# Optimization experiments

Hardware: AMD Instinct MI355X
Metric: run time of the kernel (lower is better)

The kernel has to match this reference:

```python
import jax, jax.numpy as jnp
import numpy as np

N_NODES = 50000
N_EDGES = 600000
D_NODE_IN = 32
D_EDGE_IN = 16
H = 128
D_OUT = 2
N_PASSES = 5
LN_EPS = 1e-6  # flax LayerNorm default


def _dense(key, fan_in, fan_out, scale=0.05):
    return (jax.random.normal(key, (fan_in, fan_out), dtype=jnp.float32) * scale)


def setup_inputs() -> dict:
    key = jax.random.key(0)
    ks = jax.random.split(key, 16)
    inp = {
        "nodes": jax.random.normal(ks[0], (N_NODES, D_NODE_IN), dtype=jnp.float32),
        "edges": jax.random.normal(ks[1], (N_EDGES, D_EDGE_IN), dtype=jnp.float32),
        "senders": jax.random.randint(ks[2], (N_EDGES,), 0, N_NODES, dtype=jnp.int32),
        "receivers": jax.random.randint(ks[3], (N_EDGES,), 0, N_NODES, dtype=jnp.int32),
        # node encoder ReluMLP [128,128]
        "enc_n_W0": _dense(ks[4], D_NODE_IN, H), "enc_n_b0": jnp.zeros((H,), jnp.float32),
        "enc_n_W1": _dense(ks[5], H, H), "enc_n_b1": jnp.zeros((H,), jnp.float32),
        # edge encoder ReluMLP [128,128]
        "enc_e_W0": _dense(ks[6], D_EDGE_IN, H), "enc_e_b0": jnp.zeros((H,), jnp.float32),
        "enc_e_W1": _dense(ks[7], H, H), "enc_e_b1": jnp.zeros((H,), jnp.float32),
        # weight-tied LinearMessagePassingLayer params
        "W_msg": _dense(ks[8], H + H, H),                 # Dense(no bias) on concat(sender_feat, edge)
        "node_W0": _dense(ks[9], H + H, H), "node_b0": jnp.zeros((H,), jnp.float32),
        "node_W1": _dense(ks[10], H, H), "node_b1": jnp.zeros((H,), jnp.float32),
        "W_node": _dense(ks[11], H, H),                   # residual projection, no bias
        "ln_g": jnp.ones((H,), jnp.float32), "ln_b": jnp.zeros((H,), jnp.float32),
        # node decoder ReluMLP [128,2]
        "dec_W0": _dense(ks[12], H, H), "dec_b0": jnp.zeros((H,), jnp.float32),
        "dec_W1": _dense(ks[13], H, D_OUT), "dec_b1": jnp.zeros((D_OUT,), jnp.float32),
    }
    return inp


def _relu_mlp(x, layers):
    # Dense+ReLU for all but last layer; last layer linear.
    n = len(layers)
    for i, (W, b) in enumerate(layers):
        x = x @ W + b
        if i < n - 1:
            x = jax.nn.relu(x)
    return x


def _layer_norm(x, g, b):
    mu = jnp.mean(x, axis=-1, keepdims=True)
    var = jnp.var(x, axis=-1, keepdims=True)
    return (x - mu) * jax.lax.rsqrt(var + LN_EPS) * g + b


def reference(nodes, edges, senders, receivers,
              enc_n_W0, enc_n_b0, enc_n_W1, enc_n_b1,
              enc_e_W0, enc_e_b0, enc_e_W1, enc_e_b1,
              W_msg, node_W0, node_b0, node_W1, node_b1,
              W_node, ln_g, ln_b,
              dec_W0, dec_b0, dec_W1, dec_b1):
    n = _relu_mlp(nodes, [(enc_n_W0, enc_n_b0), (enc_n_W1, enc_n_b1)])  # [N,H]
    e = _relu_mlp(edges, [(enc_e_W0, enc_e_b0), (enc_e_W1, enc_e_b1)])  # [E,H]
    total_nodes = n.shape[0]

    for _ in range(N_PASSES):  # weight-tied process block
        sender_features = n[senders]                                    # gather [E,H]
        msg_in = jnp.concatenate([sender_features, e], axis=-1)         # [E,2H]
        messages = msg_in @ W_msg                                       # [E,H]
        agg = jax.ops.segment_sum(messages, receivers, num_segments=total_nodes)
        node_in = jnp.concatenate([n, agg], axis=-1)                    # [N,2H]
        nodes_out = _relu_mlp(node_in, [(node_W0, node_b0), (node_W1, node_b1)])
        n = _layer_norm(n @ W_node + nodes_out, ln_g, ln_b)

    return _relu_mlp(n, [(dec_W0, dec_b0), (dec_W1, dec_b1)])           # [N,2]
```

## Files before the change

### kernel.cpp

```cpp
#include <hip/hip_runtime.h>

#define DEVFN __device__ __forceinline__

namespace {

constexpr int NN = 50000;
constexpr int NE = 600000;
constexpr int H  = 128;
constexpr float LN_EPS = 1e-6f;

typedef _Float16 f16x8 __attribute__((ext_vector_type(8)));
typedef _Float16 f16x4 __attribute__((ext_vector_type(4)));
typedef float f32x4 __attribute__((ext_vector_type(4)));

DEVFN void mm_block(const float* xsrow, int pitch, int K,
                    const float* __restrict__ W, int c0, float (&acc)[8][4]) {
  for (int k = 0; k < K; k += 4) {
    float4 w0 = *(const float4*)(W + (size_t)(k + 0) * H + c0);
    float4 w1 = *(const float4*)(W + (size_t)(k + 1) * H + c0);
    float4 w2 = *(const float4*)(W + (size_t)(k + 2) * H + c0);
    float4 w3 = *(const float4*)(W + (size_t)(k + 3) * H + c0);
#pragma unroll
    for (int r = 0; r < 8; ++r) {
      float4 a = *(const float4*)(xsrow + r * pitch + k);
      acc[r][0] += a.x * w0.x; acc[r][0] += a.y * w1.x; acc[r][0] += a.z * w2.x; acc[r][0] += a.w * w3.x;
      acc[r][1] += a.x * w0.y; acc[r][1] += a.y * w1.y; acc[r][1] += a.z * w2.y; acc[r][1] += a.w * w3.y;
      acc[r][2] += a.x * w0.z; acc[r][2] += a.y * w1.z; acc[r][2] += a.z * w2.z; acc[r][2] += a.w * w3.z;
      acc[r][3] += a.x * w0.w; acc[r][3] += a.y * w1.w; acc[r][3] += a.z * w2.w; acc[r][3] += a.w * w3.w;
    }
  }
}

DEVFN void linear_body(const float* __restrict__ x, const float* __restrict__ W,
                       float* __restrict__ y, int r0, int R, int t, float* xs) {
  {
    const int r = t & 31, q = t >> 5;
    int row = r0 + r;
    if (row >= R) row = R - 1;
    const float* src = &x[(size_t)row * H + q * 32];
#pragma unroll
    for (int j = 0; j < 8; ++j)
      *(float4*)&xs[r * 132 + q * 32 + j * 4] = *(const float4*)&src[j * 4];
  }
  __syncthreads();
  const int c0 = (t & 31) * 4;
  const int rbase = (t >> 5) * 8;
  float acc[8][4];
#pragma unroll
  for (int r = 0; r < 8; ++r) { acc[r][0] = 0.f; acc[r][1] = 0.f; acc[r][2] = 0.f; acc[r][3] = 0.f; }
  mm_block(&xs[rbase * 132], 132, H, W, c0, acc);
#pragma unroll
  for (int r = 0; r < 8; ++r) {
    int row = r0 + rbase + r;
    if (row < R)
      *(float4*)&y[(size_t)row * H + c0] =
          make_float4(acc[r][0], acc[r][1], acc[r][2], acc[r][3]);
  }
}

__global__ __launch_bounds__(128) void fold1_kernel(
    const float* __restrict__ Wb, const float* __restrict__ Wt,
    const float* __restrict__ W0b, float* __restrict__ T,
    float* __restrict__ Wf) {
  __shared__ float xs[32 * 132];
  const float* x = (blockIdx.x < 4) ? Wb : Wt;
  float* y = (blockIdx.x < 4) ? T : Wf;
  linear_body(x, W0b, y, (blockIdx.x & 3) * 32, 128, threadIdx.x, xs);
}

__global__ __launch_bounds__(128) void fold2_kernel(
    const float* __restrict__ W1e, const float* __restrict__ b1e,
    const float* __restrict__ T, float* __restrict__ Wc2,
    float* __restrict__ bc2) {
  __shared__ float xs[32 * 132];
  if (blockIdx.x < 4) {
    linear_body(W1e, T, Wc2, blockIdx.x * 32, 128, threadIdx.x, xs);
  } else {
    int j = threadIdx.x;
    float s = 0.f;
    for (int k = 0; k < H; ++k) s += b1e[k] * T[(size_t)k * H + j];
    bc2[j] = s;
  }
}

__global__ __launch_bounds__(64) void prepack7_kernel(
    const float* __restrict__ s0, const float* __restrict__ s1,
    const float* __restrict__ s2, const float* __restrict__ s3,
    const float* __restrict__ s4, const float* __restrict__ s5,
    const float* __restrict__ s6, _Float16* __restrict__ pkBase) {
  const int z = blockIdx.z;
  const float* W = (z == 0) ? s0 : (z == 1) ? s1 : (z == 2) ? s2 :
                   (z == 3) ? s3 : (z == 4) ? s4 : (z == 5) ? s5 : s6;
  _Float16* pk = pkBase + (size_t)z * 128 * H;
  const int ks = blockIdx.x, ct = blockIdx.y, l = threadIdx.x;
  const int kbase = ks * 32 + (l >> 4) * 8;
  const int col = ct * 16 + (l & 15);
  _Float16 tmp[8];
#pragma unroll
  for (int j = 0; j < 8; ++j)
    tmp[j] = (_Float16)W[(size_t)(kbase + j) * H + col];
  *(f16x8*)&pk[((size_t)((ks * 8 + ct) * 64) + l) * 8] = *(f16x8*)tmp;
}

__global__ __launch_bounds__(64) void prepack_w0e_kernel(
    const float* __restrict__ W0e, _Float16* __restrict__ pk) {
  const int ct = blockIdx.x, l = threadIdx.x;
  const int quad = l >> 4;
  const int col = ct * 16 + (l & 15);
  _Float16 tmp[8];
#pragma unroll
  for (int j = 0; j < 8; ++j) {
    int k = quad * 8 + j;
    tmp[j] = (quad < 2) ? (_Float16)W0e[(size_t)k * H + col] : (_Float16)0.f;
  }
  *(f16x8*)&pk[((size_t)(ct * 64) + l) * 8] = *(f16x8*)tmp;
}

__global__ __launch_bounds__(64) void prepack_k32_kernel(
    const float* __restrict__ W, _Float16* __restrict__ pk) {
  const int ct = blockIdx.x, l = threadIdx.x;
  const int quad = l >> 4;
  const int col = ct * 16 + (l & 15);
  _Float16 tmp[8];
#pragma unroll
  for (int j = 0; j < 8; ++j)
    tmp[j] = (_Float16)W[(size_t)(quad * 8 + j) * H + col];
  *(f16x8*)&pk[((size_t)(ct * 64) + l) * 8] = *(f16x8*)tmp;
}

__global__ __launch_bounds__(256) void hist_kernel(const int* __restrict__ recv,
                                                   int* __restrict__ cnt) {
  int i = blockIdx.x * 256 + threadIdx.x;
  if (i < NE) atomicAdd(&cnt[recv[i]], 1);
}

__global__ __launch_bounds__(256) void scan1_kernel(const int* __restrict__ cnt,
                                                    int* __restrict__ excl,
                                                    int* __restrict__ part) {
  __shared__ int s[256];
  int t = threadIdx.x;
  int i = blockIdx.x * 256 + t;
  int v = (i < NN) ? cnt[i] : 0;
  s[t] = v;
  __syncthreads();
  for (int off = 1; off < 256; off <<= 1) {
    int x = (t >= off) ? s[t - off] : 0;
    __syncthreads();
    s[t] += x;
    __syncthreads();
  }
  if (i < NN) excl[i] = s[t] - v;
  if (t == 255) part[blockIdx.x] = s[255];
}

__global__ __launch_bounds__(256) void scan2_kernel(int* __restrict__ part, int nb) {
  __shared__ int s[256];
  int t = threadIdx.x;
  int v = (t < nb) ? part[t] : 0;
  s[t] = v;
  __syncthreads();
  for (int off = 1; off < 256; off <<= 1) {
    int x = (t >= off) ? s[t - off] : 0;
    __syncthreads();
    s[t] += x;
    __syncthreads();
  }
  if (t < nb) part[t] = s[t] - v;
}

__global__ __launch_bounds__(256) void scan3_kernel(int* __restrict__ excl,
                                                    const int* __restrict__ part,
                                                    int* __restrict__ cursor) {
  int i = blockIdx.x * 256 + threadIdx.x;
  if (i < NN) {
    int e = excl[i] + part[i >> 8];
    excl[i] = e;
    cursor[i] = e;
  }
}

__global__ __launch_bounds__(256) void scatter_permute_kernel(
    const int* __restrict__ senders, const int* __restrict__ recv,
    int* __restrict__ cursor, const float* __restrict__ edges,
    int* __restrict__ sendp, _Float16* __restrict__ edgesP16) {
  const int t = threadIdx.x;
  const int i = blockIdx.x * 64 + (t >> 2);
  if (i >= NE) return;
  const int sub = t & 3;
  int pos = 0;
  if (sub == 0) pos = atomicAdd(&cursor[recv[i]], 1);
  pos = __shfl(pos, (t & 63) & ~3);
  if (sub == 0) sendp[pos] = senders[i];
  float4 v = *(const float4*)&edges[(size_t)i * 16 + sub * 4];
  f16x4 h = {(_Float16)v.x, (_Float16)v.y, (_Float16)v.z, (_Float16)v.w};
  *(f16x4*)&edgesP16[(size_t)pos * 16 + sub * 4] = h;
}

__global__ __launch_bounds__(256) void encoder_mfma_kernel(
    const float* __restrict__ x, const float* __restrict__ b0,
    const float* __restrict__ b1, const _Float16* __restrict__ pkEW0,
    const _Float16* __restrict__ pkEW1, _Float16* __restrict__ outp) {
  __shared__ _Float16 lds[4][16 * 136];
  const int t = threadIdx.x;
  const int wave = t >> 6, lane = t & 63;
  const int row0 = blockIdx.x * 64 + wave * 16;
  const int quad = lane >> 4, m16 = lane & 15;
  _Float16* hlds = &lds[wave][0];

  int arow = row0 + m16;
  if (arow >= NN) arow = NN - 1;
  f16x8 a0;
  {
    const float* src = &x[(size_t)arow * 32 + quad * 8];
    float4 v0 = *(const float4*)(src);
    float4 v1 = *(const float4*)(src + 4);
    a0[0] = (_Float16)v0.x; a0[1] = (_Float16)v0.y;
    a0[2] = (_Float16)v0.z; a0[3] = (_Float16)v0.w;
    a0[4] = (_Float16)v1.x; a0[5] = (_Float16)v1.y;
    a0[6] = (_Float16)v1.z; a0[7] = (_Float16)v1.w;
  }
#pragma unroll
  for (int ct = 0; ct < 8; ++ct) {
    float bb = b0[ct * 16 + m16];
    f32x4 acc = (f32x4){bb, bb, bb, bb};
    acc = __builtin_amdgcn_mfma_f32_16x16x32_f16(
        a0, *(const f16x8*)&pkEW0[((size_t)(ct * 64) + lane) * 8], acc, 0, 0, 0);
#pragma unroll
    for (int q = 0; q < 4; ++q)
      hlds[(quad * 4 + q) * 136 + ct * 16 + m16] = (_Float16)fmaxf(acc[q], 0.f);
  }
  __syncthreads();
  const _Float16* hrow = &hlds[m16 * 136 + quad * 8];
  f16x8 ah[4];
#pragma unroll
  for (int ks = 0; ks < 4; ++ks) ah[ks] = *(const f16x8*)(hrow + ks * 32);
  f32x4 acc2[8];
#pragma unroll
  for (int ct = 0; ct < 8; ++ct) {
    float bb = b1[ct * 16 + m16];
    acc2[ct] = (f32x4){bb, bb, bb, bb};
  }
#pragma unroll
  for (int ks = 0; ks < 4; ++ks) {
    const _Float16* bp = pkEW1 + ((size_t)ks * 8 * 64 + lane) * 8;
#pragma unroll
    for (int ct = 0; ct < 8; ++ct)
      acc2[ct] = __builtin_amdgcn_mfma_f32_16x16x32_f16(
          ah[ks], *(const f16x8*)(bp + ct * 512), acc2[ct], 0, 0, 0);
  }
  __syncthreads();
#pragma unroll
  for (int ct = 0; ct < 8; ++ct)
#pragma unroll
    for (int q = 0; q < 4; ++q)
      hlds[(quad * 4 + q) * 136 + ct * 16 + m16] = (_Float16)acc2[ct][q];
  __syncthreads();
  {
    int lr = lane >> 2, cc = (lane & 3) * 32;
    int orow = row0 + lr;
    if (orow < NN) {
      const _Float16* src = &hlds[lr * 136 + cc];
      _Float16* dst = &outp[(size_t)orow * H + cc];
      *(f16x8*)(dst + 0)  = *(const f16x8*)(src + 0);
      *(f16x8*)(dst + 8)  = *(const f16x8*)(src + 8);
      *(f16x8*)(dst + 16) = *(const f16x8*)(src + 16);
      *(f16x8*)(dst + 24) = *(const f16x8*)(src + 24);
    }
  }
}

__global__ __launch_bounds__(256) void hs_mfma_kernel(
    const _Float16* __restrict__ edgesP16, const int* __restrict__ start,
    const int* __restrict__ endc, const _Float16* __restrict__ pkW0e,
    const float* __restrict__ b0e, float* __restrict__ Hs) {
  const int t = threadIdx.x;
  const int wave = t >> 6, lane = t & 63;
  const int v = blockIdx.x * 4 + wave;
  const int quad = lane >> 4, m16 = lane & 15;
  const int j0 = start[v];
  const int deg = endc[v] - j0;

  float binit[8];
#pragma unroll
  for (int ct = 0; ct < 8; ++ct) binit[ct] = b0e[ct * 16 + m16];
  f16x8 bfrag[8];
#pragma unroll
  for (int ct = 0; ct < 8; ++ct)
    bfrag[ct] = *(const f16x8*)&pkW0e[((size_t)(ct * 64) + lane) * 8];

  float rsum[8][4];
#pragma unroll
  for (int ct = 0; ct < 8; ++ct)
#pragma unroll
    for (int q = 0; q < 4; ++q) rsum[ct][q] = 0.f;

  for (int base = 0; base < deg; base += 16) {
    f16x8 a = {};
    if (quad < 2 && base + m16 < deg)
      a = *(const f16x8*)&edgesP16[(size_t)(j0 + base + m16) * 16 + quad * 8];
#pragma unroll
    for (int ct = 0; ct < 8; ++ct) {
      f32x4 acc = (f32x4){binit[ct], binit[ct], binit[ct], binit[ct]};
      acc = __builtin_amdgcn_mfma_f32_16x16x32_f16(a, bfrag[ct], acc, 0, 0, 0);
#pragma unroll
      for (int q = 0; q < 4; ++q) {
        int row = quad * 4 + q;
        float hv = fmaxf(acc[q], 0.f);
        rsum[ct][q] += (base + row < deg) ? hv : 0.f;
      }
    }
  }
#pragma unroll
  for (int ct = 0; ct < 8; ++ct) {
    float s = (rsum[ct][0] + rsum[ct][1]) + (rsum[ct][2] + rsum[ct][3]);
    s += __shfl_xor(s, 16);
    s += __shfl_xor(s, 32);
    if (lane < 16) Hs[(size_t)v * H + ct * 16 + lane] = s;
  }
}

__global__ __launch_bounds__(256) void blinpack_mfma_kernel(
    const float* __restrict__ Hs, const _Float16* __restrict__ pkWc2,
    const float* __restrict__ bc2, const int* __restrict__ start,
    const int* __restrict__ endc, _Float16* __restrict__ B2pk) {
  const int t = threadIdx.x;
  const int wave = t >> 6, lane = t & 63;
  const int tile = blockIdx.x * 4 + wave;
  const int row0 = tile * 16;
  const int quad = lane >> 4, m16 = lane & 15;
  int arow = row0 + m16;
  if (arow >= NN) arow = NN - 1;
  f16x8 ah[4];
#pragma unroll
  for (int ks = 0; ks < 4; ++ks) {
    const float* src = &Hs[(size_t)arow * H + ks * 32 + quad * 8];
    float4 v0 = *(const float4*)src;
    float4 v1 = *(const float4*)(src + 4);
    f16x8 a;
    a[0] = (_Float16)v0.x; a[1] = (_Float16)v0.y;
    a[2] = (_Float16)v0.z; a[3] = (_Float16)v0.w;
    a[4] = (_Float16)v1.x; a[5] = (_Float16)v1.y;
    a[6] = (_Float16)v1.z; a[7] = (_Float16)v1.w;
    ah[ks] = a;
  }
  float degq[4];
#pragma unroll
  for (int q = 0; q < 4; ++q) {
    int r = row0 + quad * 4 + q;
    degq[q] = (r < NN) ? (float)(endc[r] - start[r]) : 0.f;
  }
  f32x4 acc[8];
#pragma unroll
  for (int ct = 0; ct < 8; ++ct) {
    float bcv = bc2[ct * 16 + m16];
    acc[ct] = (f32x4){degq[0] * bcv, degq[1] * bcv, degq[2] * bcv, degq[3] * bcv};
  }
#pragma unroll
  for (int ks = 0; ks < 4; ++ks) {
    const _Float16* bp = pkWc2 + ((size_t)ks * 8 * 64 + lane) * 8;
#pragma unroll
    for (int ct = 0; ct < 8; ++ct)
      acc[ct] = __builtin_amdgcn_mfma_f32_16x16x32_f16(
          ah[ks], *(const f16x8*)(bp + ct * 512), acc[ct], 0, 0, 0);
  }
  _Float16 tmp[32];
#pragma unroll
  for (int ct = 0; ct < 8; ++ct)
#pragma unroll
    for (int q = 0; q < 4; ++q) tmp[ct * 4 + q] = (_Float16)acc[ct][q];
  _Float16* dst = &B2pk[((size_t)tile * 64 + lane) * 32];
#pragma unroll
  for (int i = 0; i < 4; ++i)
    *(f16x8*)(dst + i * 8) = *(f16x8*)(tmp + i * 8);
}

__global__ __launch_bounds__(256) void gather_kernel(
    const _Float16* __restrict__ n16, const int* __restrict__ start,
    const int* __restrict__ endc, const int* __restrict__ sendp,
    _Float16* __restrict__ S) {
  const int t = threadIdx.x;
  const int v = blockIdx.x * 4 + (t >> 6);
  const int lane = t & 63;
  const int grp = lane >> 4;
  const int c = (lane & 15) * 8;
  float a[8] = {0.f, 0.f, 0.f, 0.f, 0.f, 0.f, 0.f, 0.f};
  const int e = endc[v];
  int j = start[v];
  for (; j + 7 < e; j += 8) {
    int s0 = sendp[j + grp];
    int s1 = sendp[j + 4 + grp];
    f16x8 p0 = *(const f16x8*)&n16[(size_t)s0 * H + c];
    f16x8 p1 = *(const f16x8*)&n16[(size_t)s1 * H + c];
#pragma unroll
    for (int i = 0; i < 8; ++i) a[i] += (float)p0[i] + (float)p1[i];
  }
  for (; j < e; j += 4) {
    int jj = j + grp;
    if (jj < e) {
      int s0 = sendp[jj];
      f16x8 p0 = *(const f16x8*)&n16[(size_t)s0 * H + c];
#pragma unroll
      for (int i = 0; i < 8; ++i) a[i] += (float)p0[i];
    }
  }
#pragma unroll
  for (int i = 0; i < 8; ++i) {
    a[i] += __shfl_xor(a[i], 16);
    a[i] += __shfl_xor(a[i], 32);
  }
  if (lane < 16) {
    f16x8 o;
#pragma unroll
    for (int i = 0; i < 8; ++i) o[i] = (_Float16)a[i];
    *(f16x8*)&S[(size_t)v * H + c] = o;
  }
}

__global__ __launch_bounds__(256) void node_mfma_kernel(
    const _Float16* __restrict__ n16, const _Float16* __restrict__ S16,
    const _Float16* __restrict__ B2pk,
    const _Float16* __restrict__ pkW0t, const _Float16* __restrict__ pkWf,
    const float* __restrict__ b0,
    const _Float16* __restrict__ pkW1, const _Float16* __restrict__ pkWn,
    const float* __restrict__ b1,
    const float* __restrict__ ln_g, const float* __restrict__ ln_b,
    _Float16* __restrict__ nout) {
  __shared__ _Float16 lds[4][16 * 136];
  const int t = threadIdx.x;
  const int wave = t >> 6, lane = t & 63;
  const int row0 = blockIdx.x * 64 + wave * 16;
  const int quad = lane >> 4, m16 = lane & 15;
  _Float16* hlds = &lds[wave][0];

  int arow = row0 + m16;
  if (arow >= NN) arow = NN - 1;
  const _Float16* nrow = &n16[(size_t)arow * H + quad * 8];
  const _Float16* srow = &S16[(size_t)arow * H + quad * 8];
  f16x8 an[4], as[4];
#pragma unroll
  for (int ks = 0; ks < 4; ++ks) {
    an[ks] = *(const f16x8*)(nrow + ks * 32);
    as[ks] = *(const f16x8*)(srow + ks * 32);
  }

  const int tile = blockIdx.x * 4 + wave;
  const _Float16* b2l = &B2pk[((size_t)tile * 64 + lane) * 32];
  f32x4 acc[8];
#pragma unroll
  for (int ct = 0; ct < 8; ++ct) {
    float bb = b0[ct * 16 + m16];
    f16x4 bv = *(const f16x4*)(b2l + ct * 4);
    acc[ct] = (f32x4){bb + (float)bv[0], bb + (float)bv[1],
                      bb + (float)bv[2], bb + (float)bv[3]};
  }
#pragma unroll
  for (int ks = 0; ks < 4; ++ks) {
    const _Float16* bp0 = pkW0t + ((size_t)ks * 8 * 64 + lane) * 8;
    const _Float16* bpf = pkWf + ((size_t)ks * 8 * 64 + lane) * 8;
#pragma unroll
    for (int ct = 0; ct < 8; ++ct) {
      f16x8 bw0 = *(const f16x8*)(bp0 + ct * 512);
      acc[ct] = __builtin_amdgcn_mfma_f32_16x16x32_f16(an[ks], bw0, acc[ct], 0, 0, 0);
      f16x8 bwf = *(const f16x8*)(bpf + ct * 512);
      acc[ct] = __builtin_amdgcn_mfma_f32_16x16x32_f16(as[ks], bwf, acc[ct], 0, 0, 0);
    }
  }
#pragma unroll
  for (int ct = 0; ct < 8; ++ct) {
#pragma unroll
    for (int q = 0; q < 4; ++q)
      hlds[(quad * 4 + q) * 136 + ct * 16 + m16] =
          (_Float16)fmaxf(acc[ct][q], 0.f);
  }
  __syncthreads();

  const _Float16* hrow = &hlds[m16 * 136 + quad * 8];
  f32x4 acc2[8];
#pragma unroll
  for (int ct = 0; ct < 8; ++ct) {
    float bb = b1[ct * 16 + m16];
    acc2[ct] = (f32x4){bb, bb, bb, bb};
  }
#pragma unroll
  for (int ks = 0; ks < 4; ++ks) {
    f16x8 ah = *(const f16x8*)(hrow + ks * 32);
    const _Float16* bp1 = pkW1 + ((size_t)ks * 8 * 64 + lane) * 8;
    const _Float16* bpn = pkWn + ((size_t)ks * 8 * 64 + lane) * 8;
#pragma unroll
    for (int ct = 0; ct < 8; ++ct) {
      f16x8 b1f = *(const f16x8*)(bp1 + ct * 512);
      acc2[ct] = __builtin_amdgcn_mfma_f32_16x16x32_f16(ah, b1f, acc2[ct], 0, 0, 0);
      f16x8 bnf = *(const f16x8*)(bpn + ct * 512);
      acc2[ct] = __builtin_amdgcn_mfma_f32_16x16x32_f16(an[ks], bnf, acc2[ct], 0, 0, 0);
    }
  }

  float gv[8], bv[8];
#pragma unroll
  for (int ct = 0; ct < 8; ++ct) {
    gv[ct] = ln_g[ct * 16 + m16];
    bv[ct] = ln_b[ct * 16 + m16];
  }
  __syncthreads();
#pragma unroll
  for (int q = 0; q < 4; ++q) {
    float s1 = 0.f, s2 = 0.f;
#pragma unroll
    for (int ct = 0; ct < 8; ++ct) {
      float v = acc2[ct][q];
      s1 += v; s2 += v * v;
    }
#pragma unroll
    for (int m = 1; m <= 8; m <<= 1) {
      s1 += __shfl_xor(s1, m);
      s2 += __shfl_xor(s2, m);
    }
    float mu = s1 * (1.f / 128.f);
    float var = s2 * (1.f / 128.f) - mu * mu;
    float rs = rsqrtf(var + LN_EPS);
#pragma unroll
    for (int ct = 0; ct < 8; ++ct) {
      float o = (acc2[ct][q] - mu) * rs * gv[ct] + bv[ct];
      hlds[(quad * 4 + q) * 136 + ct * 16 + m16] = (_Float16)o;
    }
  }
  __syncthreads();

  {
    int lr = lane >> 2;
    int cc = (lane & 3) * 32;
    const _Float16* src = &hlds[lr * 136 + cc];
    int orow = row0 + lr;
    if (orow < NN) {
      _Float16* dst = &nout[(size_t)orow * H + cc];
      *(f16x8*)(dst + 0)  = *(const f16x8*)(src + 0);
      *(f16x8*)(dst + 8)  = *(const f16x8*)(src + 8);
      *(f16x8*)(dst + 16) = *(const f16x8*)(src + 16);
      *(f16x8*)(dst + 24) = *(const f16x8*)(src + 24);
    }
  }
}

__global__ __launch_bounds__(256) void decode_mfma_kernel(
    const _Float16* __restrict__ n, const float* __restrict__ b0,
    const _Float16* __restrict__ pkDW0, const float* __restrict__ W1,
    const float* __restrict__ b1, float* __restrict__ out) {
  const int t = threadIdx.x;
  const int wave = t >> 6, lane = t & 63;
  const int row0 = blockIdx.x * 64 + wave * 16;
  const int quad = lane >> 4, m16 = lane & 15;
  int arow = row0 + m16;
  if (arow >= NN) arow = NN - 1;
  const _Float16* nrow = &n[(size_t)arow * H + quad * 8];
  f16x8 an[4];
#pragma unroll
  for (int ks = 0; ks < 4; ++ks) an[ks] = *(const f16x8*)(nrow + ks * 32);
  f32x4 acc[8];
#pragma unroll
  for (int ct = 0; ct < 8; ++ct) {
    float bb = b0[ct * 16 + m16];
    acc[ct] = (f32x4){bb, bb, bb, bb};
  }
#pragma unroll
  for (int ks = 0; ks < 4; ++ks) {
    const _Float16* bp = pkDW0 + ((size_t)ks * 8 * 64 + lane) * 8;
#pragma unroll
    for (int ct = 0; ct < 8; ++ct)
      acc[ct] = __builtin_amdgcn_mfma_f32_16x16x32_f16(
          an[ks], *(const f16x8*)(bp + ct * 512), acc[ct], 0, 0, 0);
  }
  float s0[4] = {0.f, 0.f, 0.f, 0.f}, s1[4] = {0.f, 0.f, 0.f, 0.f};
#pragma unroll
  for (int ct = 0; ct < 8; ++ct) {
    const float2 w = *(const float2*)&W1[(size_t)(ct * 16 + m16) * 2];
#pragma unroll
    for (int q = 0; q < 4; ++q) {
      float h = fmaxf(acc[ct][q], 0.f);
      s0[q] += h * w.x;
      s1[q] += h * w.y;
    }
  }
#pragma unroll
  for (int q = 0; q < 4; ++q) {
#pragma unroll
    for (int m = 1; m <= 8; m <<= 1) {
      s0[q] += __shfl_xor(s0[q], m);
      s1[q] += __shfl_xor(s1[q], m);
    }
  }
  if (m16 == 0) {
#pragma unroll
    for (int q = 0; q < 4; ++q) {
      int r = row0 + quad * 4 + q;
      if (r < NN) {
        out[(size_t)r * 2 + 0] = s0[q] + b1[0];
        out[(size_t)r * 2 + 1] = s1[q] + b1[1];
      }
    }
  }
}

__global__ __launch_bounds__(256) void zero_kernel(float4* __restrict__ p, int n4) {
  int i = blockIdx.x * 256 + threadIdx.x;
  if (i < n4) p[i] = make_float4(0.f, 0.f, 0.f, 0.f);
}

}

extern "C" void kernel_launch(void* const* d_in, const int* in_sizes, int n_in,
                              void* d_out, int out_size, void* d_ws, size_t ws_size,
                              hipStream_t stream) {
  const float* nodes     = (const float*)d_in[0];
  const float* edges     = (const float*)d_in[1];
  const int*   senders   = (const int*)d_in[2];
  const int*   receivers = (const int*)d_in[3];
  const float* enc_n_W0 = (const float*)d_in[4];
  const float* enc_n_b0 = (const float*)d_in[5];
  const float* enc_n_W1 = (const float*)d_in[6];
  const float* enc_n_b1 = (const float*)d_in[7];
  const float* enc_e_W0 = (const float*)d_in[8];
  const float* enc_e_b0 = (const float*)d_in[9];
  const float* enc_e_W1 = (const float*)d_in[10];
  const float* enc_e_b1 = (const float*)d_in[11];
  const float* W_msg    = (const float*)d_in[12];
  const float* node_W0  = (const float*)d_in[13];
  const float* node_b0  = (const float*)d_in[14];
  const float* node_W1  = (const float*)d_in[15];
  const float* node_b1  = (const float*)d_in[16];
  const float* W_node   = (const float*)d_in[17];
  const float* ln_g     = (const float*)d_in[18];
  const float* ln_b     = (const float*)d_in[19];
  const float* dec_W0   = (const float*)d_in[20];
  const float* dec_b0   = (const float*)d_in[21];
  const float* dec_W1   = (const float*)d_in[22];
  const float* dec_b1   = (const float*)d_in[23];
  float* out = (float*)d_out;

  const float* Wt  = W_msg;
  const float* Wb  = W_msg + 128 * H;
  const float* W0t = node_W0;
  const float* W0b = node_W0 + 128 * H;

  const int mfmaBlocks = (NN + 63) / 64;
  const int nTiles     = mfmaBlocks * 4;

  float* Hs     = (float*)d_ws;
  float* T      = Hs + (size_t)NN * H;
  float* Wc2    = T + 128 * H;
  float* Wf32   = Wc2 + 128 * H;
  float* bc2    = Wf32 + 128 * H;
  _Float16* edgesP16 = (_Float16*)(bc2 + 128);
  _Float16* n16a  = edgesP16 + (size_t)NE * 16;
  _Float16* n16b  = n16a + (size_t)NN * H;
  _Float16* S16   = n16b + (size_t)NN * H;
  _Float16* B2pk  = S16 + (size_t)NN * H;
  _Float16* pkAll = B2pk + (size_t)nTiles * 64 * 32;
  _Float16* pkW0t = pkAll;
  _Float16* pkWf  = pkAll + 1 * 128 * H;
  _Float16* pkW1  = pkAll + 2 * 128 * H;
  _Float16* pkWn  = pkAll + 3 * 128 * H;
  _Float16* pkEW1 = pkAll + 4 * 128 * H;
  _Float16* pkDW0 = pkAll + 5 * 128 * H;
  _Float16* pkWc2 = pkAll + 6 * 128 * H;
  _Float16* pkW0e = pkAll + 7 * 128 * H;
  _Float16* pkEW0 = pkW0e + 4096;
  int* cnt    = (int*)(pkEW0 + 4096);
  int* excl   = cnt + NN;
  int* cursor = excl + NN;
  int* part   = cursor + NN;
  int* sendp  = part + 256;

  const int scanBlocks = (NN + 255) / 256;
  const int neBlocks   = (NE + 255) / 256;

  zero_kernel<<<(NN / 4 + 255) / 256, 256, 0, stream>>>((float4*)cnt, NN / 4);
  hist_kernel<<<neBlocks, 256, 0, stream>>>(receivers, cnt);
  scan1_kernel<<<scanBlocks, 256, 0, stream>>>(cnt, excl, part);
  scan2_kernel<<<1, 256, 0, stream>>>(part, scanBlocks);
  scan3_kernel<<<scanBlocks, 256, 0, stream>>>(excl, part, cursor);
  scatter_permute_kernel<<<(NE + 63) / 64, 256, 0, stream>>>(
      senders, receivers, cursor, edges, sendp, edgesP16);

  fold1_kernel<<<8, 128, 0, stream>>>(Wb, Wt, W0b, T, Wf32);
  fold2_kernel<<<5, 128, 0, stream>>>(enc_e_W1, enc_e_b1, T, Wc2, bc2);
  prepack7_kernel<<<dim3(4, 8, 7), 64, 0, stream>>>(
      W0t, Wf32, node_W1, W_node, enc_n_W1, dec_W0, Wc2, pkAll);
  prepack_w0e_kernel<<<8, 64, 0, stream>>>(enc_e_W0, pkW0e);
  prepack_k32_kernel<<<8, 64, 0, stream>>>(enc_n_W0, pkEW0);

  encoder_mfma_kernel<<<mfmaBlocks, 256, 0, stream>>>(
      nodes, enc_n_b0, enc_n_b1, pkEW0, pkEW1, n16a);
  hs_mfma_kernel<<<NN / 4, 256, 0, stream>>>(
      edgesP16, excl, cursor, pkW0e, enc_e_b0, Hs);
  blinpack_mfma_kernel<<<mfmaBlocks, 256, 0, stream>>>(
      Hs, pkWc2, bc2, excl, cursor, B2pk);

  _Float16* ncur = n16a;
  _Float16* nnxt = n16b;
  for (int p = 0; p < 5; ++p) {
    gather_kernel<<<NN / 4, 256, 0, stream>>>(ncur, excl, cursor, sendp, S16);
    node_mfma_kernel<<<mfmaBlocks, 256, 0, stream>>>(
        ncur, S16, B2pk, pkW0t, pkWf, node_b0, pkW1, pkWn, node_b1,
        ln_g, ln_b, nnxt);
    _Float16* tmp = ncur; ncur = nnxt; nnxt = tmp;
  }

  decode_mfma_kernel<<<mfmaBlocks, 256, 0, stream>>>(
      ncur, dec_b0, pkDW0, dec_W1, dec_b1, out);
}
```

Before: 559.9 us.

## Fuse edge-encoder hidden sum and bilinear pack into one kernel via LDS

Merges the per-node edge hidden-sum kernel and the following MFMA projection/pack kernel into one kernel. Each block handles a 16-node tile, stages the fp16 hidden sums in shared memory, then does the projection, so the fp32 Hs intermediate in global memory is no longer written and read back. The edge bias is folded into the packed weights through a constant-one input column, which removes the per-row validity masking. Shared-memory staging now rounds the hidden sums to fp16 before the second GEMM, the same as before. A small zero kernel clears the padded tail tiles.

```diff
diff --git a/kernel.cpp b/kernel.cpp
--- a/kernel.cpp
+++ b/kernel.cpp
@@ -103,7 +103,8 @@
 }
 
 __global__ __launch_bounds__(64) void prepack_w0e_kernel(
-    const float* __restrict__ W0e, _Float16* __restrict__ pk) {
+    const float* __restrict__ W0e, const float* __restrict__ b0e,
+    _Float16* __restrict__ pk) {
   const int ct = blockIdx.x, l = threadIdx.x;
   const int quad = l >> 4;
   const int col = ct * 16 + (l & 15);
@@ -111,7 +112,8 @@
 #pragma unroll
   for (int j = 0; j < 8; ++j) {
     int k = quad * 8 + j;
-    tmp[j] = (quad < 2) ? (_Float16)W0e[(size_t)k * H + col] : (_Float16)0.f;
+    float v = (quad < 2) ? W0e[(size_t)k * H + col] : (k == 16 ? b0e[col] : 0.f);
+    tmp[j] = (_Float16)v;
   }
   *(f16x8*)&pk[((size_t)(ct * 64) + l) * 8] = *(f16x8*)tmp;
 }
@@ -269,109 +271,96 @@
   }
 }
 
-__global__ __launch_bounds__(256) void hs_mfma_kernel(
+__global__ __launch_bounds__(256) void hsblin_kernel(
     const _Float16* __restrict__ edgesP16, const int* __restrict__ start,
     const int* __restrict__ endc, const _Float16* __restrict__ pkW0e,
-    const float* __restrict__ b0e, float* __restrict__ Hs) {
+    const _Float16* __restrict__ pkWc2, const float* __restrict__ bc2,
+    _Float16* __restrict__ B2pk) {
+  __shared__ _Float16 hl[16][136];
+  __shared__ float degl[16];
   const int t = threadIdx.x;
   const int wave = t >> 6, lane = t & 63;
-  const int v = blockIdx.x * 4 + wave;
   const int quad = lane >> 4, m16 = lane & 15;
-  const int j0 = start[v];
-  const int deg = endc[v] - j0;
-
-  float binit[8];
-#pragma unroll
-  for (int ct = 0; ct < 8; ++ct) binit[ct] = b0e[ct * 16 + m16];
+  const int tile = blockIdx.x;
+
   f16x8 bfrag[8];
 #pragma unroll
   for (int ct = 0; ct < 8; ++ct)
     bfrag[ct] = *(const f16x8*)&pkW0e[((size_t)(ct * 64) + lane) * 8];
 
-  float rsum[8][4];
-#pragma unroll
-  for (int ct = 0; ct < 8; ++ct)
-#pragma unroll
-    for (int q = 0; q < 4; ++q) rsum[ct][q] = 0.f;
-
-  for (int base = 0; base < deg; base += 16) {
-    f16x8 a = {};
-    if (quad < 2 && base + m16 < deg)
-      a = *(const f16x8*)&edgesP16[(size_t)(j0 + base + m16) * 16 + quad * 8];
+  for (int k = 0; k < 4; ++k) {
+    const int v = tile * 16 + wave * 4 + k;
+    const int j0 = start[v];
+    const int deg = endc[v] - j0;
+    float rsum[8][4];
+#pragma unroll
+    for (int ct = 0; ct < 8; ++ct)
+#pragma unroll
+      for (int q = 0; q < 4; ++q) rsum[ct][q] = 0.f;
+    for (int base = 0; base < deg; base += 16) {
+      const bool valid = (base + m16 < deg);
+      f16x8 a = {};
+      if (quad < 2) {
+        if (valid)
+          a = *(const f16x8*)&edgesP16[(size_t)(j0 + base + m16) * 16 + quad * 8];
+      } else if (quad == 2) {
+        a[0] = valid ? (_Float16)1.f : (_Float16)0.f;
+      }
+#pragma unroll
+      for (int ct = 0; ct < 8; ++ct) {
+        f32x4 acc = (f32x4){0.f, 0.f, 0.f, 0.f};
+        acc = __builtin_amdgcn_mfma_f32_16x16x32_f16(a, bfrag[ct], acc, 0, 0, 0);
+#pragma unroll
+        for (int q = 0; q < 4; ++q) rsum[ct][q] += fmaxf(acc[q], 0.f);
+      }
+    }
 #pragma unroll
     for (int ct = 0; ct < 8; ++ct) {
-      f32x4 acc = (f32x4){binit[ct], binit[ct], binit[ct], binit[ct]};
-      acc = __builtin_amdgcn_mfma_f32_16x16x32_f16(a, bfrag[ct], acc, 0, 0, 0);
-#pragma unroll
-      for (int q = 0; q < 4; ++q) {
-        int row = quad * 4 + q;
-        float hv = fmaxf(acc[q], 0.f);
-        rsum[ct][q] += (base + row < deg) ? hv : 0.f;
-      }
-    }
-  }
-#pragma unroll
-  for (int ct = 0; ct < 8; ++ct) {
-    float s = (rsum[ct][0] + rsum[ct][1]) + (rsum[ct][2] + rsum[ct][3]);
-    s += __shfl_xor(s, 16);
-    s += __shfl_xor(s, 32);
-    if (lane < 16) Hs[(size_t)v * H + ct * 16 + lane] = s;
-  }
-}
-
-__global__ __launch_bounds__(256) void blinpack_mfma_kernel(
-    const float* __restrict__ Hs, const _Float16* __restrict__ pkWc2,
-    const float* __restrict__ bc2, const int* __restrict__ start,
-    const int* __restrict__ endc, _Float16* __restrict__ B2pk) {
-  const int t = threadIdx.x;
-  const int wave = t >> 6, lane = t & 63;
-  const int tile = blockIdx.x * 4 + wave;
-  const int row0 = tile * 16;
-  const int quad = lane >> 4, m16 = lane & 15;
-  int arow = row0 + m16;
-  if (arow >= NN) arow = NN - 1;
+      float s = (rsum[ct][0] + rsum[ct][1]) + (rsum[ct][2] + rsum[ct][3]);
+      s += __shfl_xor(s, 16);
+      s += __shfl_xor(s, 32);
+      rsum[ct][0] = s;
+    }
+    const int nl = wave * 4 + k;
+#pragma unroll
+    for (int i = 0; i < 2; ++i) {
+      int ct = quad * 2 + i;
+      hl[nl][ct * 16 + m16] = (_Float16)rsum[ct][0];
+    }
+    if (lane == 0) degl[nl] = (float)deg;
+  }
+  __syncthreads();
+
   f16x8 ah[4];
 #pragma unroll
+  for (int ks = 0; ks < 4; ++ks)
+    ah[ks] = *(const f16x8*)&hl[m16][ks * 32 + quad * 8];
+  float degq[4];
+#pragma unroll
+  for (int q = 0; q < 4; ++q) degq[q] = degl[quad * 4 + q];
+  f32x4 acc[2];
+#pragma unroll
+  for (int i = 0; i < 2; ++i) {
+    int ct = wave * 2 + i;
+    float bcv = bc2[ct * 16 + m16];
+    acc[i] = (f32x4){degq[0] * bcv, degq[1] * bcv, degq[2] * bcv, degq[3] * bcv};
+  }
+#pragma unroll
   for (int ks = 0; ks < 4; ++ks) {
-    const float* src = &Hs[(size_t)arow * H + ks * 32 + quad * 8];
-    float4 v0 = *(const float4*)src;
-    float4 v1 = *(const float4*)(src + 4);
-    f16x8 a;
-    a[0] = (_Float16)v0.x; a[1] = (_Float16)v0.y;
-    a[2] = (_Float16)v0.z; a[3] = (_Float16)v0.w;
-    a[4] = (_Float16)v1.x; a[5] = (_Float16)v1.y;
-    a[6] = (_Float16)v1.z; a[7] = (_Float16)v1.w;
-    ah[ks] = a;
-  }
-  float degq[4];
-#pragma unroll
-  for (int q = 0; q < 4; ++q) {
-    int r = row0 + quad * 4 + q;
-    degq[q] = (r < NN) ? (float)(endc[r] - start[r]) : 0.f;
-  }
-  f32x4 acc[8];
-#pragma unroll
-  for (int ct = 0; ct < 8; ++ct) {
-    float bcv = bc2[ct * 16 + m16];
-    acc[ct] = (f32x4){degq[0] * bcv, degq[1] * bcv, degq[2] * bcv, degq[3] * bcv};
-  }
-#pragma unroll
-  for (int ks = 0; ks < 4; ++ks) {
-    const _Float16* bp = pkWc2 + ((size_t)ks * 8 * 64 + lane) * 8;
-#pragma unroll
-    for (int ct = 0; ct < 8; ++ct)
-      acc[ct] = __builtin_amdgcn_mfma_f32_16x16x32_f16(
-          ah[ks], *(const f16x8*)(bp + ct * 512), acc[ct], 0, 0, 0);
-  }
-  _Float16 tmp[32];
-#pragma unroll
-  for (int ct = 0; ct < 8; ++ct)
-#pragma unroll
-    for (int q = 0; q < 4; ++q) tmp[ct * 4 + q] = (_Float16)acc[ct][q];
-  _Float16* dst = &B2pk[((size_t)tile * 64 + lane) * 32];
-#pragma unroll
-  for (int i = 0; i < 4; ++i)
-    *(f16x8*)(dst + i * 8) = *(f16x8*)(tmp + i * 8);
+#pragma unroll
+    for (int i = 0; i < 2; ++i) {
+      int ct = wave * 2 + i;
+      const _Float16* bp = pkWc2 + ((size_t)((ks * 8 + ct) * 64) + lane) * 8;
+      acc[i] = __builtin_amdgcn_mfma_f32_16x16x32_f16(
+          ah[ks], *(const f16x8*)bp, acc[i], 0, 0, 0);
+    }
+  }
+  _Float16 tmp[8];
+#pragma unroll
+  for (int i = 0; i < 2; ++i)
+#pragma unroll
+    for (int q = 0; q < 4; ++q) tmp[i * 4 + q] = (_Float16)acc[i][q];
+  *(f16x8*)&B2pk[((size_t)tile * 64 + lane) * 32 + wave * 8] = *(f16x8*)tmp;
 }
 
 __global__ __launch_bounds__(256) void gather_kernel(
@@ -643,9 +632,9 @@
 
   const int mfmaBlocks = (NN + 63) / 64;
   const int nTiles     = mfmaBlocks * 4;
-
-  float* Hs     = (float*)d_ws;
-  float* T      = Hs + (size_t)NN * H;
+  const int hsTiles    = NN / 16;
+
+  float* T      = (float*)d_ws;
   float* Wc2    = T + 128 * H;
   float* Wf32   = Wc2 + 128 * H;
   float* bc2    = Wf32 + 128 * H;
@@ -685,15 +674,15 @@
   fold2_kernel<<<5, 128, 0, stream>>>(enc_e_W1, enc_e_b1, T, Wc2, bc2);
   prepack7_kernel<<<dim3(4, 8, 7), 64, 0, stream>>>(
       W0t, Wf32, node_W1, W_node, enc_n_W1, dec_W0, Wc2, pkAll);
-  prepack_w0e_kernel<<<8, 64, 0, stream>>>(enc_e_W0, pkW0e);
+  prepack_w0e_kernel<<<8, 64, 0, stream>>>(enc_e_W0, enc_e_b0, pkW0e);
   prepack_k32_kernel<<<8, 64, 0, stream>>>(enc_n_W0, pkEW0);
 
   encoder_mfma_kernel<<<mfmaBlocks, 256, 0, stream>>>(
       nodes, enc_n_b0, enc_n_b1, pkEW0, pkEW1, n16a);
-  hs_mfma_kernel<<<NN / 4, 256, 0, stream>>>(
-      edgesP16, excl, cursor, pkW0e, enc_e_b0, Hs);
-  blinpack_mfma_kernel<<<mfmaBlocks, 256, 0, stream>>>(
-      Hs, pkWc2, bc2, excl, cursor, B2pk);
+  zero_kernel<<<3, 256, 0, stream>>>(
+      (float4*)(B2pk + (size_t)hsTiles * 64 * 32), (nTiles - hsTiles) * 512);
+  hsblin_kernel<<<hsTiles, 256, 0, stream>>>(
+      edgesP16, excl, cursor, pkW0e, pkWc2, bc2, B2pk);
 
   _Float16* ncur = n16a;
   _Float16* nnxt = n16b;
```

Result: no change. 562.1 us (+0.4%).
